# Kernel optimization log

Measured on AMD Instinct MI355X. Metric: run time of the kernel, lower is better.

## Reference

```python
import jax, jax.numpy as jnp
import numpy as np

SOFTENING = 0.01
SOFTENING_SQ = SOFTENING * SOFTENING


def setup_inputs() -> dict:
    key = jax.random.key(0)
    k1, k2 = jax.random.split(key)
    N = 8192
    positions = jax.random.normal(k1, (N, 3), dtype=jnp.float32)
    masses = jax.random.uniform(k2, (N,), dtype=jnp.float32)
    return {"positions": positions, "masses": masses}


def reference(positions, masses):
    # diff[i, j] = r_j - r_i  -> shape (N, N, 3)
    diff = positions[None, :, :] - positions[:, None, :]
    dist_sq = jnp.sum(diff * diff, axis=2) + SOFTENING_SQ        # (N, N)
    inv_dist_cubed = dist_sq ** (-1.5)                            # (N, N)
    # a_i = sum_j m_j * diff[i, j] * inv_dist_cubed[i, j]
    w = masses[None, :] * inv_dist_cubed                          # (N, N)
    accelerations = jnp.einsum('ij,ijd->id', w, diff)             # (N, 3)
    return accelerations
```

## Files before the change

### kernel.cpp

```cpp
#include <hip/hip_runtime.h>

#define NBODY 8192
#define BLOCK 256
#define SLABS 32
#define JCHUNK (NBODY / SLABS)
#define SOFT2 1.0e-4f

__global__ __launch_bounds__(BLOCK) void nbody_kernel(
    const float* __restrict__ pos, const float* __restrict__ mass,
    float* __restrict__ out) {
  __shared__ float4 tile[JCHUNK];

  const int t = threadIdx.x;
  const int i = blockIdx.x * BLOCK + t;
  const int j0 = blockIdx.y * JCHUNK;

  const int j = j0 + t;
  tile[t] = make_float4(pos[j * 3 + 0], pos[j * 3 + 1], pos[j * 3 + 2],
                        mass[j]);

  const float xi = pos[i * 3 + 0];
  const float yi = pos[i * 3 + 1];
  const float zi = pos[i * 3 + 2];

  __syncthreads();

  float ax = 0.f, ay = 0.f, az = 0.f;
#pragma unroll 8
  for (int k = 0; k < JCHUNK; ++k) {
    float4 o = tile[k];
    float dx = o.x - xi;
    float dy = o.y - yi;
    float dz = o.z - zi;
    float r2 = fmaf(dx, dx, fmaf(dy, dy, fmaf(dz, dz, SOFT2)));
    float inv = __builtin_amdgcn_rsqf(r2);
    float w = o.w * (inv * inv * inv);
    ax = fmaf(w, dx, ax);
    ay = fmaf(w, dy, ay);
    az = fmaf(w, dz, az);
  }

  atomicAdd(&out[i * 3 + 0], ax);
  atomicAdd(&out[i * 3 + 1], ay);
  atomicAdd(&out[i * 3 + 2], az);
}

extern "C" void kernel_launch(void* const* d_in, const int* in_sizes, int n_in,
                              void* d_out, int out_size, void* d_ws,
                              size_t ws_size, hipStream_t stream) {
  const float* pos = (const float*)d_in[0];
  const float* mass = (const float*)d_in[1];
  float* out = (float*)d_out;

  hipMemsetAsync(d_out, 0, (size_t)out_size * sizeof(float), stream);

  dim3 grid(NBODY / BLOCK, SLABS);
  nbody_kernel<<<grid, BLOCK, 0, stream>>>(pos, mass, out);
}
```

Before: 78.66 us.

## Split into pack, two-bodies-per-thread force, and deterministic slab reduction kernels

Packs positions and masses into float4 once, then has each thread accumulate two i-bodies and read j-bodies straight from global memory (a wave-uniform broadcast) instead of a shared-memory tile. The j-range is split into 64 slabs whose partial sums go to workspace and are summed by a third kernel, replacing the memset and atomics. This aims to raise ILP and reuse each loaded j-body across two i-bodies, while cutting atomic traffic and shared-memory syncs. The cost is two extra kernel launches, workspace traffic for the partial sums, and fewer blocks per slab.

```diff
diff --git a/kernel.cpp b/kernel.cpp
--- a/kernel.cpp
+++ b/kernel.cpp
@@ -2,47 +2,72 @@
 
 #define NBODY 8192
 #define BLOCK 256
-#define SLABS 32
+#define IPT 2
+#define ITILE (BLOCK * IPT)
+#define NITILES (NBODY / ITILE)
+#define SLABS 64
 #define JCHUNK (NBODY / SLABS)
+#define NF (NBODY * 3)
 #define SOFT2 1.0e-4f
 
-__global__ __launch_bounds__(BLOCK) void nbody_kernel(
+__global__ __launch_bounds__(BLOCK) void pack_kernel(
     const float* __restrict__ pos, const float* __restrict__ mass,
-    float* __restrict__ out) {
-  __shared__ float4 tile[JCHUNK];
+    float4* __restrict__ pw) {
+  const int i = blockIdx.x * BLOCK + threadIdx.x;
+  pw[i] = make_float4(pos[i * 3 + 0], pos[i * 3 + 1], pos[i * 3 + 2], mass[i]);
+}
 
+__global__ __launch_bounds__(BLOCK) void force_kernel(
+    const float4* __restrict__ pw, float* __restrict__ part) {
   const int t = threadIdx.x;
-  const int i = blockIdx.x * BLOCK + t;
-  const int j0 = blockIdx.y * JCHUNK;
+  const int i1 = blockIdx.x * ITILE + t;
+  const int i2 = i1 + BLOCK;
+  const int jbase = blockIdx.y * JCHUNK;
 
-  const int j = j0 + t;
-  tile[t] = make_float4(pos[j * 3 + 0], pos[j * 3 + 1], pos[j * 3 + 2],
-                        mass[j]);
+  const float4 p1 = pw[i1];
+  const float4 p2 = pw[i2];
+  const float x1 = p1.x, y1 = p1.y, z1 = p1.z;
+  const float x2 = p2.x, y2 = p2.y, z2 = p2.z;
 
-  const float xi = pos[i * 3 + 0];
-  const float yi = pos[i * 3 + 1];
-  const float zi = pos[i * 3 + 2];
+  float ax1 = 0.f, ay1 = 0.f, az1 = 0.f;
+  float ax2 = 0.f, ay2 = 0.f, az2 = 0.f;
 
-  __syncthreads();
-
-  float ax = 0.f, ay = 0.f, az = 0.f;
 #pragma unroll 8
   for (int k = 0; k < JCHUNK; ++k) {
-    float4 o = tile[k];
-    float dx = o.x - xi;
-    float dy = o.y - yi;
-    float dz = o.z - zi;
-    float r2 = fmaf(dx, dx, fmaf(dy, dy, fmaf(dz, dz, SOFT2)));
-    float inv = __builtin_amdgcn_rsqf(r2);
-    float w = o.w * (inv * inv * inv);
-    ax = fmaf(w, dx, ax);
-    ay = fmaf(w, dy, ay);
-    az = fmaf(w, dz, az);
+    const float4 o = pw[jbase + k];
+
+    float dx1 = o.x - x1, dy1 = o.y - y1, dz1 = o.z - z1;
+    float dx2 = o.x - x2, dy2 = o.y - y2, dz2 = o.z - z2;
+    float r21 = fmaf(dx1, dx1, fmaf(dy1, dy1, fmaf(dz1, dz1, SOFT2)));
+    float r22 = fmaf(dx2, dx2, fmaf(dy2, dy2, fmaf(dz2, dz2, SOFT2)));
+    float in1 = __builtin_amdgcn_rsqf(r21);
+    float in2 = __builtin_amdgcn_rsqf(r22);
+    float w1 = o.w * (in1 * in1 * in1);
+    float w2 = o.w * (in2 * in2 * in2);
+    ax1 = fmaf(w1, dx1, ax1);
+    ay1 = fmaf(w1, dy1, ay1);
+    az1 = fmaf(w1, dz1, az1);
+    ax2 = fmaf(w2, dx2, ax2);
+    ay2 = fmaf(w2, dy2, ay2);
+    az2 = fmaf(w2, dz2, az2);
   }
 
-  atomicAdd(&out[i * 3 + 0], ax);
-  atomicAdd(&out[i * 3 + 1], ay);
-  atomicAdd(&out[i * 3 + 2], az);
+  float* __restrict__ dst = part + (size_t)blockIdx.y * NF;
+  dst[i1 * 3 + 0] = ax1;
+  dst[i1 * 3 + 1] = ay1;
+  dst[i1 * 3 + 2] = az1;
+  dst[i2 * 3 + 0] = ax2;
+  dst[i2 * 3 + 1] = ay2;
+  dst[i2 * 3 + 2] = az2;
+}
+
+__global__ __launch_bounds__(BLOCK) void reduce_kernel(
+    const float* __restrict__ part, float* __restrict__ out) {
+  const int idx = blockIdx.x * BLOCK + threadIdx.x;
+  float s = 0.f;
+#pragma unroll
+  for (int sl = 0; sl < SLABS; ++sl) s += part[(size_t)sl * NF + idx];
+  out[idx] = s;
 }
 
 extern "C" void kernel_launch(void* const* d_in, const int* in_sizes, int n_in,
@@ -52,8 +77,10 @@
   const float* mass = (const float*)d_in[1];
   float* out = (float*)d_out;
 
-  hipMemsetAsync(d_out, 0, (size_t)out_size * sizeof(float), stream);
+  float4* pw = (float4*)d_ws;
+  float* part = (float*)d_ws + (size_t)NBODY * 4;
 
-  dim3 grid(NBODY / BLOCK, SLABS);
-  nbody_kernel<<<grid, BLOCK, 0, stream>>>(pos, mass, out);
+  pack_kernel<<<NBODY / BLOCK, BLOCK, 0, stream>>>(pos, mass, pw);
+  force_kernel<<<dim3(NITILES, SLABS), BLOCK, 0, stream>>>(pw, part);
+  reduce_kernel<<<NF / BLOCK, BLOCK, 0, stream>>>(part, out);
 }
```

Measured after the change: 96.28 us. 22.4% more time.
